# Kernel optimization log

Measured on AMD Instinct MI355X. Metric: run time of the kernel, lower is better.

The kernel has to match this reference:

```python
import jax, jax.numpy as jnp
import numpy as np

N_NODES = 100000

def setup_inputs() -> dict:
    key = jax.random.key(0)
    k1, k2, k3, k4, k5, k6 = jax.random.split(key, 6)
    input = jax.random.normal(k1, (N_NODES, 256), dtype=jnp.float32)
    weight = jax.random.normal(k2, (256, 256), dtype=jnp.float32) * (1.0 / np.sqrt(256))
    bias = jax.random.normal(k3, (256,), dtype=jnp.float32) * 0.02
    edge_rows = jax.random.randint(k4, (3200000,), 0, N_NODES, dtype=jnp.int32)
    edge_cols = jax.random.randint(k5, (3200000,), 0, N_NODES, dtype=jnp.int32)
    edge_vals = jax.random.uniform(k6, (3200000,), dtype=jnp.float32)
    return {"input": input, "weight": weight, "bias": bias,
            "edge_rows": edge_rows, "edge_cols": edge_cols, "edge_vals": edge_vals}

def reference(input, weight, bias, edge_rows, edge_cols, edge_vals):
    # support = X @ W  -- dense GEMM [N, in] x [in, out]
    support = input @ weight
    # output = spmm(adj, support): out[r] += adj[r,c] * support[c]
    gathered = support[edge_cols] * edge_vals[:, None]          # [E, out]
    output = jax.ops.segment_sum(gathered, edge_rows, num_segments=N_NODES)
    return output + bias
```

## Files before the change

kernel.cpp:

```cpp
#include <hip/hip_runtime.h>
#include <hip/hip_bf16.h>
#include <stdint.h>

#define M_NODES 100000
#define DIM     256
#define N_EDGES 3200000
#define CAP     80
#define CHUNK   8192
#define NWG1    391
#define NB      391
#define BCAP    9216

typedef __bf16 bf16x8 __attribute__((ext_vector_type(8)));
typedef float  f32x4  __attribute__((ext_vector_type(4)));
typedef unsigned short u16x8 __attribute__((ext_vector_type(8)));

__device__ __forceinline__ unsigned short f2bf(float f) {
    unsigned u = __float_as_uint(f);
    u += 0x7FFF + ((u >> 16) & 1);
    return (unsigned short)(u >> 16);
}
__device__ __forceinline__ float bf2f(unsigned short h) {
    return __uint_as_float(((unsigned)h) << 16);
}

__global__ __launch_bounds__(256) void k_convert_wt(const float* __restrict__ W,
                                                    unsigned short* __restrict__ Wt,
                                                    int* __restrict__ cur) {
    int k = blockIdx.x, n = threadIdx.x;
    Wt[n * 256 + k] = f2bf(W[k * 256 + n]);
    int gid = k * 256 + n;
    if (gid < NB) cur[gid] = 0;
}

__global__ __launch_bounds__(256) void k_gemm(const float* __restrict__ X,
                                              const unsigned short* __restrict__ Wt,
                                              unsigned short* __restrict__ Sb) {
    int wave = threadIdx.x >> 6;
    int lane = threadIdx.x & 63;
    int tile = blockIdx.x * 4 + wave;
    if (tile >= M_NODES / 16) return;
    int m0   = tile * 16;
    int quad = lane >> 4;
    int r    = lane & 15;

    const float* aptr = X + (size_t)(m0 + r) * 256 + quad * 8;

    f32x4 acc[16];
#pragma unroll
    for (int t = 0; t < 16; ++t) acc[t] = {0.f, 0.f, 0.f, 0.f};

#pragma unroll
    for (int k0 = 0; k0 < 256; k0 += 32) {
        f32x4 a0 = *(const f32x4*)(aptr + k0);
        f32x4 a1 = *(const f32x4*)(aptr + k0 + 4);
        unsigned short au[8];
        au[0] = f2bf(a0.x); au[1] = f2bf(a0.y); au[2] = f2bf(a0.z); au[3] = f2bf(a0.w);
        au[4] = f2bf(a1.x); au[5] = f2bf(a1.y); au[6] = f2bf(a1.z); au[7] = f2bf(a1.w);
        bf16x8 a = *(bf16x8*)au;
#pragma unroll
        for (int t = 0; t < 16; ++t) {
            bf16x8 b = *(const bf16x8*)(Wt + (size_t)(t * 16 + r) * 256 + k0 + quad * 8);
            acc[t] = __builtin_amdgcn_mfma_f32_16x16x32_bf16(a, b, acc[t], 0, 0, 0);
        }
    }

#pragma unroll
    for (int t = 0; t < 16; ++t)
#pragma unroll
        for (int i = 0; i < 4; ++i)
            Sb[(size_t)(m0 + quad * 4 + i) * 256 + t * 16 + r] = f2bf(acc[t][i]);
}

__global__ __launch_bounds__(512) void k_part2(const int* __restrict__ rows,
                                               const int* __restrict__ cols,
                                               const float* __restrict__ vals,
                                               uint64_t* __restrict__ part,
                                               int* __restrict__ cur) {
    __shared__ int cnt[NB];
    __shared__ int wcur[NB];
    int w = blockIdx.x, t = threadIdx.x;
    int base = w * CHUNK;
    int clen = N_EDGES - base; if (clen > CHUNK) clen = CHUNK;

    for (int i = t; i < NB; i += 512) cnt[i] = 0;
    __syncthreads();
    for (int i = t; i < clen; i += 512)
        atomicAdd(&cnt[rows[base + i] >> 8], 1);
    __syncthreads();

    for (int b = t; b < NB; b += 512)
        wcur[b] = atomicAdd(&cur[b], cnt[b]);
    __syncthreads();

    for (int i = t; i < clen; i += 512) {
        int   r = rows[base + i];
        int   c = cols[base + i];
        float v = vals[base + i];
        int   b = r >> 8;
        int pos = atomicAdd(&wcur[b], 1);
        if (pos < BCAP) {
            uint32_t lo = (uint32_t)c | ((uint32_t)(r & 255) << 17);
            part[(size_t)b * BCAP + pos] = ((uint64_t)__float_as_uint(v) << 32) | lo;
        }
    }
}

__global__ __launch_bounds__(512) void k_build3(const uint64_t* __restrict__ part,
                                                const int* __restrict__ cur,
                                                uint32_t* __restrict__ csr4,
                                                int* __restrict__ counts) {
    __shared__ int lcnt[256];
    int b = blockIdx.x, t = threadIdx.x;
    if (t < 256) lcnt[t] = 0;
    int n = cur[b];
    if (n > BCAP) n = BCAP;
    __syncthreads();

    const uint64_t* p = part + (size_t)b * BCAP;
    for (int i = t; i < n; i += 512) {
        uint64_t ent = p[i];
        uint32_t lo  = (uint32_t)ent;
        int   rl = (lo >> 17) & 255;
        int   c  = lo & 0x1FFFF;
        float v  = __uint_as_float((uint32_t)(ent >> 32));
        int qv = (int)(v * 32768.f + 0.5f);
        if (qv > 32767) qv = 32767;
        int pos = atomicAdd(&lcnt[rl], 1);
        if (pos < CAP)
            csr4[(size_t)(b * 256 + rl) * CAP + pos] = ((uint32_t)c << 15) | (uint32_t)qv;
    }
    __syncthreads();
    if (t < 256) counts[b * 256 + t] = lcnt[t];
}

__global__ __launch_bounds__(256) void k_spmm(const int* __restrict__ counts,
                                              const uint32_t* __restrict__ csr4,
                                              const unsigned short* __restrict__ Sb,
                                              const float* __restrict__ bias,
                                              float* __restrict__ out) {
    int wave = threadIdx.x >> 6;
    int lane = threadIdx.x & 63;
    int r = blockIdx.x * 4 + wave;
    if (r >= M_NODES) return;
    int n = counts[r];
    if (n > CAP) n = CAP;
    const uint32_t* ep = csr4 + (size_t)r * CAP;
    int half = lane >> 5;
    int l    = lane & 31;

    float acc[8] = {0.f, 0.f, 0.f, 0.f, 0.f, 0.f, 0.f, 0.f};
    int j = 0;
    for (; j + 7 < n; j += 8) {
        uint32_t m0 = ep[j +     half];
        uint32_t m1 = ep[j + 2 + half];
        uint32_t m2 = ep[j + 4 + half];
        uint32_t m3 = ep[j + 6 + half];
        int c0 = m0 >> 15;  float v0 = (float)(m0 & 0x7FFF) * (1.f / 32768.f);
        int c1 = m1 >> 15;  float v1 = (float)(m1 & 0x7FFF) * (1.f / 32768.f);
        int c2 = m2 >> 15;  float v2 = (float)(m2 & 0x7FFF) * (1.f / 32768.f);
        int c3 = m3 >> 15;  float v3 = (float)(m3 & 0x7FFF) * (1.f / 32768.f);
        u16x8 s0 = *(const u16x8*)(Sb + (size_t)c0 * 256 + l * 8);
        u16x8 s1 = *(const u16x8*)(Sb + (size_t)c1 * 256 + l * 8);
        u16x8 s2 = *(const u16x8*)(Sb + (size_t)c2 * 256 + l * 8);
        u16x8 s3 = *(const u16x8*)(Sb + (size_t)c3 * 256 + l * 8);
#pragma unroll
        for (int i = 0; i < 8; ++i) acc[i] += bf2f(s0[i]) * v0;
#pragma unroll
        for (int i = 0; i < 8; ++i) acc[i] += bf2f(s1[i]) * v1;
#pragma unroll
        for (int i = 0; i < 8; ++i) acc[i] += bf2f(s2[i]) * v2;
#pragma unroll
        for (int i = 0; i < 8; ++i) acc[i] += bf2f(s3[i]) * v3;
    }
    for (; j + 1 < n; j += 2) {
        uint32_t m0 = ep[j + half];
        int c0 = m0 >> 15;  float v0 = (float)(m0 & 0x7FFF) * (1.f / 32768.f);
        u16x8 s0 = *(const u16x8*)(Sb + (size_t)c0 * 256 + l * 8);
#pragma unroll
        for (int i = 0; i < 8; ++i) acc[i] += bf2f(s0[i]) * v0;
    }
    if (j < n && half == 0) {
        uint32_t m0 = ep[j];
        int c0 = m0 >> 15;  float v0 = (float)(m0 & 0x7FFF) * (1.f / 32768.f);
        u16x8 s0 = *(const u16x8*)(Sb + (size_t)c0 * 256 + l * 8);
#pragma unroll
        for (int i = 0; i < 8; ++i) acc[i] += bf2f(s0[i]) * v0;
    }

#pragma unroll
    for (int i = 0; i < 8; ++i) acc[i] += __shfl(acc[i], lane + 32);

    if (half == 0) {
        f32x4 b0 = *(const f32x4*)(bias + l * 8);
        f32x4 b1 = *(const f32x4*)(bias + l * 8 + 4);
        f32x4 o0 = {acc[0] + b0.x, acc[1] + b0.y, acc[2] + b0.z, acc[3] + b0.w};
        f32x4 o1 = {acc[4] + b1.x, acc[5] + b1.y, acc[6] + b1.z, acc[7] + b1.w};
        float* op = out + (size_t)r * 256 + l * 8;
        *(f32x4*)op       = o0;
        *(f32x4*)(op + 4) = o1;
    }
}

extern "C" void kernel_launch(void* const* d_in, const int* in_sizes, int n_in,
                              void* d_out, int out_size, void* d_ws, size_t ws_size,
                              hipStream_t stream) {
    const float* X    = (const float*)d_in[0];
    const float* W    = (const float*)d_in[1];
    const float* bias = (const float*)d_in[2];
    const int*   er   = (const int*)d_in[3];
    const int*   ec   = (const int*)d_in[4];
    const float* ev   = (const float*)d_in[5];
    float* out = (float*)d_out;

    char* ws = (char*)d_ws;
    unsigned short* Wt     = (unsigned short*)ws;
    uint32_t*       csr4   = (uint32_t*)(ws + 131072);
    int*            cur    = (int*)(ws + 32161792);
    int*            counts = (int*)(ws + 32166912);
    uint64_t*       part   = (uint64_t*)(ws + 32567296);
    unsigned short* Sb     = (unsigned short*)(ws + 32567296);

    k_convert_wt<<<256,   256, 0, stream>>>(W, Wt, cur);
    k_part2     <<<NWG1,  512, 0, stream>>>(er, ec, ev, part, cur);
    k_build3    <<<NB,    512, 0, stream>>>(part, cur, csr4, counts);
    k_gemm      <<<1563,  256, 0, stream>>>(X, Wt, Sb);
    k_spmm      <<<25000, 256, 0, stream>>>(counts, csr4, Sb, bias, out);
}
```

Baseline: 615.0 us.

## Replace two-pass bucketed CSR build with direct atomics; stage W in LDS for GEMM

The two-kernel bucket partition plus local sort is replaced by a single kernel that builds the CSR with global atomics on per-row counters, which removes the intermediate partition buffer and one pass over the edges. The GEMM now stages the transposed bf16 weight into swizzled shared memory in two K halves and has each wave compute 32 rows instead of 16, so weight reads are reused from LDS rather than refetched from global memory. The cost is more global atomic contention in the build and a larger register footprint in the GEMM from the 32 accumulators.

```diff
diff --git a/kernel.cpp b/kernel.cpp
--- a/kernel.cpp
+++ b/kernel.cpp
@@ -6,10 +6,8 @@
 #define DIM     256
 #define N_EDGES 3200000
 #define CAP     80
-#define CHUNK   8192
-#define NWG1    391
-#define NB      391
-#define BCAP    9216
+#define NGB     782
+#define NBB     1563
 
 typedef __bf16 bf16x8 __attribute__((ext_vector_type(8)));
 typedef float  f32x4  __attribute__((ext_vector_type(4)));
@@ -26,112 +24,105 @@
 
 __global__ __launch_bounds__(256) void k_convert_wt(const float* __restrict__ W,
                                                     unsigned short* __restrict__ Wt,
-                                                    int* __restrict__ cur) {
+                                                    int* __restrict__ counts) {
     int k = blockIdx.x, n = threadIdx.x;
     Wt[n * 256 + k] = f2bf(W[k * 256 + n]);
     int gid = k * 256 + n;
-    if (gid < NB) cur[gid] = 0;
+    for (int i = gid; i < M_NODES + 96; i += 256 * 256) counts[i] = 0;
+}
+
+__global__ __launch_bounds__(256) void k_build(const int* __restrict__ rows,
+                                               const int* __restrict__ cols,
+                                               const float* __restrict__ vals,
+                                               uint32_t* __restrict__ csr4,
+                                               int* __restrict__ counts) {
+    int base = blockIdx.x * 2048;
+#pragma unroll
+    for (int u = 0; u < 8; ++u) {
+        int i = base + u * 256 + threadIdx.x;
+        if (i < N_EDGES) {
+            int   r = rows[i];
+            int   c = cols[i];
+            float v = vals[i];
+            int q = (int)(v * 32768.f + 0.5f);
+            if (q > 32767) q = 32767;
+            int pos = atomicAdd(&counts[r], 1);
+            if (pos < CAP)
+                csr4[(size_t)r * CAP + pos] = ((uint32_t)c << 15) | (uint32_t)q;
+        }
+    }
 }
 
 __global__ __launch_bounds__(256) void k_gemm(const float* __restrict__ X,
                                               const unsigned short* __restrict__ Wt,
                                               unsigned short* __restrict__ Sb) {
-    int wave = threadIdx.x >> 6;
-    int lane = threadIdx.x & 63;
-    int tile = blockIdx.x * 4 + wave;
-    if (tile >= M_NODES / 16) return;
-    int m0   = tile * 16;
+    __shared__ unsigned short wlds[32768];
+    int t    = threadIdx.x;
+    int wave = t >> 6;
+    int lane = t & 63;
     int quad = lane >> 4;
     int r    = lane & 15;
-
-    const float* aptr = X + (size_t)(m0 + r) * 256 + quad * 8;
-
-    f32x4 acc[16];
-#pragma unroll
-    for (int t = 0; t < 16; ++t) acc[t] = {0.f, 0.f, 0.f, 0.f};
-
-#pragma unroll
-    for (int k0 = 0; k0 < 256; k0 += 32) {
-        f32x4 a0 = *(const f32x4*)(aptr + k0);
-        f32x4 a1 = *(const f32x4*)(aptr + k0 + 4);
-        unsigned short au[8];
-        au[0] = f2bf(a0.x); au[1] = f2bf(a0.y); au[2] = f2bf(a0.z); au[3] = f2bf(a0.w);
-        au[4] = f2bf(a1.x); au[5] = f2bf(a1.y); au[6] = f2bf(a1.z); au[7] = f2bf(a1.w);
-        bf16x8 a = *(bf16x8*)au;
-#pragma unroll
-        for (int t = 0; t < 16; ++t) {
-            bf16x8 b = *(const bf16x8*)(Wt + (size_t)(t * 16 + r) * 256 + k0 + quad * 8);
-            acc[t] = __builtin_amdgcn_mfma_f32_16x16x32_bf16(a, b, acc[t], 0, 0, 0);
-        }
-    }
-
-#pragma unroll
-    for (int t = 0; t < 16; ++t)
-#pragma unroll
-        for (int i = 0; i < 4; ++i)
-            Sb[(size_t)(m0 + quad * 4 + i) * 256 + t * 16 + r] = f2bf(acc[t][i]);
-}
-
-__global__ __launch_bounds__(512) void k_part2(const int* __restrict__ rows,
-                                               const int* __restrict__ cols,
-                                               const float* __restrict__ vals,
-                                               uint64_t* __restrict__ part,
-                                               int* __restrict__ cur) {
-    __shared__ int cnt[NB];
-    __shared__ int wcur[NB];
-    int w = blockIdx.x, t = threadIdx.x;
-    int base = w * CHUNK;
-    int clen = N_EDGES - base; if (clen > CHUNK) clen = CHUNK;
-
-    for (int i = t; i < NB; i += 512) cnt[i] = 0;
-    __syncthreads();
-    for (int i = t; i < clen; i += 512)
-        atomicAdd(&cnt[rows[base + i] >> 8], 1);
-    __syncthreads();
-
-    for (int b = t; b < NB; b += 512)
-        wcur[b] = atomicAdd(&cur[b], cnt[b]);
-    __syncthreads();
-
-    for (int i = t; i < clen; i += 512) {
-        int   r = rows[base + i];
-        int   c = cols[base + i];
-        float v = vals[base + i];
-        int   b = r >> 8;
-        int pos = atomicAdd(&wcur[b], 1);
-        if (pos < BCAP) {
-            uint32_t lo = (uint32_t)c | ((uint32_t)(r & 255) << 17);
-            part[(size_t)b * BCAP + pos] = ((uint64_t)__float_as_uint(v) << 32) | lo;
-        }
-    }
-}
-
-__global__ __launch_bounds__(512) void k_build3(const uint64_t* __restrict__ part,
-                                                const int* __restrict__ cur,
-                                                uint32_t* __restrict__ csr4,
-                                                int* __restrict__ counts) {
-    __shared__ int lcnt[256];
-    int b = blockIdx.x, t = threadIdx.x;
-    if (t < 256) lcnt[t] = 0;
-    int n = cur[b];
-    if (n > BCAP) n = BCAP;
-    __syncthreads();
-
-    const uint64_t* p = part + (size_t)b * BCAP;
-    for (int i = t; i < n; i += 512) {
-        uint64_t ent = p[i];
-        uint32_t lo  = (uint32_t)ent;
-        int   rl = (lo >> 17) & 255;
-        int   c  = lo & 0x1FFFF;
-        float v  = __uint_as_float((uint32_t)(ent >> 32));
-        int qv = (int)(v * 32768.f + 0.5f);
-        if (qv > 32767) qv = 32767;
-        int pos = atomicAdd(&lcnt[rl], 1);
-        if (pos < CAP)
-            csr4[(size_t)(b * 256 + rl) * CAP + pos] = ((uint32_t)c << 15) | (uint32_t)qv;
-    }
-    __syncthreads();
-    if (t < 256) counts[b * 256 + t] = lcnt[t];
+    int m0   = blockIdx.x * 128 + wave * 32;
+
+    int rowA = m0 + r;       if (rowA >= M_NODES) rowA = M_NODES - 1;
+    int rowB = m0 + 16 + r;  if (rowB >= M_NODES) rowB = M_NODES - 1;
+    const float* apA = X + (size_t)rowA * 256;
+    const float* apB = X + (size_t)rowB * 256;
+
+    f32x4 acc[32];
+#pragma unroll
+    for (int i = 0; i < 32; ++i) acc[i] = {0.f, 0.f, 0.f, 0.f};
+
+    for (int kh = 0; kh < 2; ++kh) {
+        if (kh) __syncthreads();
+#pragma unroll
+        for (int it = 0; it < 16; ++it) {
+            int f   = it * 256 + t;
+            int row = f >> 4;
+            int ci  = f & 15;
+            u16x8 v = *(const u16x8*)(Wt + row * 256 + kh * 128 + ci * 8);
+            int lb  = (row * 256 + ci * 16) ^ ((row & 7) << 4);
+            *(u16x8*)((char*)wlds + lb) = v;
+        }
+        __syncthreads();
+
+#pragma unroll
+        for (int ks = 0; ks < 4; ++ks) {
+            int k0 = kh * 128 + ks * 32;
+            f32x4 a0 = *(const f32x4*)(apA + k0 + quad * 8);
+            f32x4 a1 = *(const f32x4*)(apA + k0 + quad * 8 + 4);
+            f32x4 b0 = *(const f32x4*)(apB + k0 + quad * 8);
+            f32x4 b1 = *(const f32x4*)(apB + k0 + quad * 8 + 4);
+            unsigned short au[8], bu[8];
+            au[0]=f2bf(a0.x); au[1]=f2bf(a0.y); au[2]=f2bf(a0.z); au[3]=f2bf(a0.w);
+            au[4]=f2bf(a1.x); au[5]=f2bf(a1.y); au[6]=f2bf(a1.z); au[7]=f2bf(a1.w);
+            bu[0]=f2bf(b0.x); bu[1]=f2bf(b0.y); bu[2]=f2bf(b0.z); bu[3]=f2bf(b0.w);
+            bu[4]=f2bf(b1.x); bu[5]=f2bf(b1.y); bu[6]=f2bf(b1.z); bu[7]=f2bf(b1.w);
+            bf16x8 aA = *(bf16x8*)au;
+            bf16x8 aB = *(bf16x8*)bu;
+            int lcol = ks * 64 + quad * 16;
+#pragma unroll
+            for (int tt = 0; tt < 16; ++tt) {
+                int row = tt * 16 + r;
+                int lb  = (row * 256 + lcol) ^ ((row & 7) << 4);
+                bf16x8 b = *(const bf16x8*)((char*)wlds + lb);
+                acc[tt]      = __builtin_amdgcn_mfma_f32_16x16x32_bf16(aA, b, acc[tt],      0, 0, 0);
+                acc[16 + tt] = __builtin_amdgcn_mfma_f32_16x16x32_bf16(aB, b, acc[16 + tt], 0, 0, 0);
+            }
+        }
+    }
+
+#pragma unroll
+    for (int tt = 0; tt < 16; ++tt)
+#pragma unroll
+        for (int i = 0; i < 4; ++i) {
+            int ra = m0 + quad * 4 + i;
+            if (ra < M_NODES)
+                Sb[(size_t)ra * 256 + tt * 16 + r] = f2bf(acc[tt][i]);
+            int rb = m0 + 16 + quad * 4 + i;
+            if (rb < M_NODES)
+                Sb[(size_t)rb * 256 + tt * 16 + r] = f2bf(acc[16 + tt][i]);
+        }
 }
 
 __global__ __launch_bounds__(256) void k_spmm(const int* __restrict__ counts,
@@ -216,14 +207,11 @@
     char* ws = (char*)d_ws;
     unsigned short* Wt     = (unsigned short*)ws;
     uint32_t*       csr4   = (uint32_t*)(ws + 131072);
-    int*            cur    = (int*)(ws + 32161792);
-    int*            counts = (int*)(ws + 32166912);
-    uint64_t*       part   = (uint64_t*)(ws + 32567296);
-    unsigned short* Sb     = (unsigned short*)(ws + 32567296);
-
-    k_convert_wt<<<256,   256, 0, stream>>>(W, Wt, cur);
-    k_part2     <<<NWG1,  512, 0, stream>>>(er, ec, ev, part, cur);
-    k_build3    <<<NB,    512, 0, stream>>>(part, cur, csr4, counts);
-    k_gemm      <<<1563,  256, 0, stream>>>(X, Wt, Sb);
+    int*            counts = (int*)(ws + 32161792);
+    unsigned short* Sb     = (unsigned short*)(ws + 32562176);
+
+    k_convert_wt<<<256,   256, 0, stream>>>(W, Wt, counts);
+    k_build     <<<NBB,   256, 0, stream>>>(er, ec, ev, csr4, counts);
+    k_gemm      <<<NGB,   256, 0, stream>>>(X, Wt, Sb);
     k_spmm      <<<25000, 256, 0, stream>>>(counts, csr4, Sb, bias, out);
 }
```

Result: no change. 621.5 us (+1.1%).
